# Kernel tuning notes

Measured on AMD Instinct MI355X. Metric: run time of the kernel, lower is better.

The kernel has to match this reference:

```python
import jax, jax.numpy as jnp
import numpy as np
from jax.scipy.special import logsumexp

N_ALPHA = 8192
N_BETA = 8192
N_LAYERS = 16


def setup_inputs() -> dict:
    key = jax.random.key(0)
    k1, k2, k3 = jax.random.split(key, 3)
    alpha = jax.random.uniform(k1, (N_ALPHA,), jnp.float32, 1e-3, 1.0)
    alpha = alpha / alpha.sum()
    beta = jax.random.uniform(k2, (N_BETA,), jnp.float32, 1e-3, 1.0)
    beta = beta / beta.sum()
    C = jax.random.uniform(k3, (N_ALPHA, N_BETA), jnp.float32, 0.0, 1.0)
    eps = jnp.float32(0.1)
    return {"alpha": alpha, "beta": beta, "C": C, "eps": eps}


def reference(alpha, beta, C, eps):
    # Log-domain Sinkhorn iterations (tol=None -> run all n_layers).
    log_alpha = jnp.log(alpha)
    log_beta = jnp.log(beta)

    def step(carry, _):
        _, g = carry
        # log_dot_exp(C, g, eps): logsumexp over n_beta axis of (-C + g[None,:]) / eps
        f = eps * (log_alpha - logsumexp((g[None, :] - C) / eps, axis=-1))
        # log_dot_exp(C.T, f, eps): logsumexp over n_alpha axis of (-C + f[:,None]) / eps
        g_new = eps * (log_beta - logsumexp((f[:, None] - C) / eps, axis=0))
        return (f, g_new), None

    init = (jnp.zeros_like(alpha), jnp.zeros_like(beta))
    (f, g), _ = jax.lax.scan(step, init, None, length=N_LAYERS)
    return f, g
```

## Files before the change

kernel.cpp:

```cpp
#include <hip/hip_runtime.h>

#define NA 8192
#define NB 8192
#define N_LAYERS 16
#define ROWS_PER_VC 64
#define N_VC (NA / ROWS_PER_VC)

typedef _Float16 half_t;
typedef _Float16 half8_t __attribute__((ext_vector_type(8)));
typedef float float4_t __attribute__((ext_vector_type(4)));

template <bool WRITE_E>
__global__ __launch_bounds__(256) void sink_u_first(
    const float* __restrict__ C, const float* __restrict__ alpha,
    const float* __restrict__ d_eps, half_t* __restrict__ E,
    float* __restrict__ u)
{
    const int row = blockIdx.x;
    const int t = threadIdx.x;
    const float inv_eps = 1.0f / d_eps[0];
    const float4_t* Crow = (const float4_t*)(C + (size_t)row * NB);
    half8_t* Erow = (half8_t*)(E + (size_t)row * NB);

    float s = 0.0f;
#pragma unroll
    for (int k = 0; k < 4; ++k) {
        const int g = k * 256 + t;
        float4_t c0 = Crow[2 * g];
        float4_t c1 = Crow[2 * g + 1];
        float e0 = __expf(-c0.x * inv_eps);
        float e1 = __expf(-c0.y * inv_eps);
        float e2 = __expf(-c0.z * inv_eps);
        float e3 = __expf(-c0.w * inv_eps);
        float e4 = __expf(-c1.x * inv_eps);
        float e5 = __expf(-c1.y * inv_eps);
        float e6 = __expf(-c1.z * inv_eps);
        float e7 = __expf(-c1.w * inv_eps);
        if (WRITE_E) {
            half8_t h;
            h[0] = (_Float16)e0; h[1] = (_Float16)e1;
            h[2] = (_Float16)e2; h[3] = (_Float16)e3;
            h[4] = (_Float16)e4; h[5] = (_Float16)e5;
            h[6] = (_Float16)e6; h[7] = (_Float16)e7;
            Erow[g] = h;
        }
        s += ((e0 + e1) + (e2 + e3)) + ((e4 + e5) + (e6 + e7));
    }

    __shared__ float sm[256];
    sm[t] = s;
    __syncthreads();
    for (int off = 128; off > 0; off >>= 1) {
        if (t < off) sm[t] += sm[t + off];
        __syncthreads();
    }
    if (t == 0) u[row] = alpha[row] / sm[0];
}

template <bool USE_E>
__global__ __launch_bounds__(256) void sink_u_step(
    const void* __restrict__ mat, const float* __restrict__ v,
    const float* __restrict__ alpha, const float* __restrict__ d_eps,
    float* __restrict__ u)
{
    const int row = blockIdx.x;
    const int t = threadIdx.x;
    const float4_t* vv = (const float4_t*)v;
    float s = 0.0f;

    if (USE_E) {
        const half8_t* Erow = (const half8_t*)mat + (size_t)row * (NB / 8);
#pragma unroll
        for (int k = 0; k < 4; ++k) {
            const int g = k * 256 + t;
            half8_t e = Erow[g];
            float4_t w0 = vv[2 * g], w1 = vv[2 * g + 1];
            s += (float)e[0] * w0.x + (float)e[1] * w0.y +
                 (float)e[2] * w0.z + (float)e[3] * w0.w;
            s += (float)e[4] * w1.x + (float)e[5] * w1.y +
                 (float)e[6] * w1.z + (float)e[7] * w1.w;
        }
    } else {
        const float inv_eps = 1.0f / d_eps[0];
        const float4_t* Crow = (const float4_t*)mat + (size_t)row * (NB / 4);
#pragma unroll
        for (int k = 0; k < 8; ++k) {
            const int g = k * 256 + t;
            float4_t c = Crow[g];
            float4_t w = vv[g];
            s += __expf(-c.x * inv_eps) * w.x + __expf(-c.y * inv_eps) * w.y +
                 __expf(-c.z * inv_eps) * w.z + __expf(-c.w * inv_eps) * w.w;
        }
    }

    __shared__ float sm[256];
    sm[t] = s;
    __syncthreads();
    for (int off = 128; off > 0; off >>= 1) {
        if (t < off) sm[t] += sm[t + off];
        __syncthreads();
    }
    if (t == 0) u[row] = alpha[row] / sm[0];
}

template <bool USE_E>
__global__ __launch_bounds__(256) void sink_v_partial(
    const void* __restrict__ mat, const float* __restrict__ u,
    const float* __restrict__ d_eps, float* __restrict__ partial)
{
    const int cc = blockIdx.x;
    const int rc = blockIdx.y;
    const int t = threadIdx.x;
    const int row0 = rc * ROWS_PER_VC;

    float acc[8];
#pragma unroll
    for (int k = 0; k < 8; ++k) acc[k] = 0.0f;

    if (USE_E) {
        const half8_t* Eb = (const half8_t*)mat;
        const int g = cc * 256 + t;
#pragma unroll 8
        for (int r = 0; r < ROWS_PER_VC; ++r) {
            const float ur = u[row0 + r];
            half8_t e = Eb[(size_t)(row0 + r) * (NB / 8) + g];
#pragma unroll
            for (int k = 0; k < 8; ++k) acc[k] += ur * (float)e[k];
        }
    } else {
        const float inv_eps = 1.0f / d_eps[0];
        const float4_t* Cb = (const float4_t*)mat;
        const int g = (cc * 256 + t) * 2;
#pragma unroll 4
        for (int r = 0; r < ROWS_PER_VC; ++r) {
            const float ur = u[row0 + r];
            float4_t c0 = Cb[(size_t)(row0 + r) * (NB / 4) + g];
            float4_t c1 = Cb[(size_t)(row0 + r) * (NB / 4) + g + 1];
            acc[0] += ur * __expf(-c0.x * inv_eps);
            acc[1] += ur * __expf(-c0.y * inv_eps);
            acc[2] += ur * __expf(-c0.z * inv_eps);
            acc[3] += ur * __expf(-c0.w * inv_eps);
            acc[4] += ur * __expf(-c1.x * inv_eps);
            acc[5] += ur * __expf(-c1.y * inv_eps);
            acc[6] += ur * __expf(-c1.z * inv_eps);
            acc[7] += ur * __expf(-c1.w * inv_eps);
        }
    }

    float4_t o0 = {acc[0], acc[1], acc[2], acc[3]};
    float4_t o1 = {acc[4], acc[5], acc[6], acc[7]};
    float4_t* p = (float4_t*)(partial + (size_t)rc * NB + (size_t)(cc * 256 + t) * 8);
    p[0] = o0;
    p[1] = o1;
}

__global__ __launch_bounds__(256) void sink_v_combine(
    const float* __restrict__ partial, const float* __restrict__ beta,
    float* __restrict__ v)
{
    const int col = blockIdx.x * 256 + threadIdx.x;
    float s = 0.0f;
#pragma unroll 8
    for (int rc = 0; rc < N_VC; ++rc) s += partial[(size_t)rc * NB + col];
    v[col] = beta[col] / s;
}

__global__ __launch_bounds__(256) void sink_finalize(
    const float* __restrict__ u, const float* __restrict__ v,
    const float* __restrict__ d_eps, float* __restrict__ out)
{
    const int i = blockIdx.x * 256 + threadIdx.x;
    const float eps = d_eps[0];
    if (i < NA) {
        out[i] = eps * logf(u[i]);
    } else if (i < NA + NB) {
        out[i] = eps * logf(v[i - NA]);
    }
}

extern "C" void kernel_launch(void* const* d_in, const int* in_sizes, int n_in,
                              void* d_out, int out_size, void* d_ws, size_t ws_size,
                              hipStream_t stream)
{
    const float* alpha = (const float*)d_in[0];
    const float* beta  = (const float*)d_in[1];
    const float* C     = (const float*)d_in[2];
    const float* d_eps = (const float*)d_in[3];
    float* out = (float*)d_out;

    const size_t eBytes = (size_t)NA * NB * sizeof(half_t);
    const size_t pBytes = (size_t)N_VC * NB * sizeof(float);
    const size_t vecBytes = (size_t)NA * sizeof(float);

    char* ws = (char*)d_ws;
    const bool useE = ws_size >= eBytes + pBytes + 2 * vecBytes;

    size_t off = 0;
    half_t* E = nullptr;
    if (useE) { E = (half_t*)ws; off += eBytes; }
    float* partial = (float*)(ws + off); off += pBytes;
    float* u = (float*)(ws + off); off += vecBytes;
    float* v = (float*)(ws + off); off += vecBytes;

    const dim3 blk(256);
    const dim3 gridRow(NA);
    const dim3 gridVP(NB / 2048, N_VC);
    const dim3 gridVC(NB / 256);

    for (int layer = 0; layer < N_LAYERS; ++layer) {
        if (layer == 0) {
            if (useE)
                sink_u_first<true><<<gridRow, blk, 0, stream>>>(C, alpha, d_eps, E, u);
            else
                sink_u_first<false><<<gridRow, blk, 0, stream>>>(C, alpha, d_eps, nullptr, u);
        } else {
            if (useE)
                sink_u_step<true><<<gridRow, blk, 0, stream>>>(E, v, alpha, d_eps, u);
            else
                sink_u_step<false><<<gridRow, blk, 0, stream>>>(C, v, alpha, d_eps, u);
        }
        if (useE)
            sink_v_partial<true><<<gridVP, blk, 0, stream>>>(E, u, d_eps, partial);
        else
            sink_v_partial<false><<<gridVP, blk, 0, stream>>>(C, u, d_eps, partial);
        sink_v_combine<<<gridVC, blk, 0, stream>>>(partial, beta, v);
    }
    sink_finalize<<<dim3((NA + NB) / 256), blk, 0, stream>>>(u, v, d_eps, out);
}
```

Baseline: 1.166 ms.

## Fuse all Sinkhorn layers into one cooperative persistent kernel with grid syncs

Replaces the roughly 49 separate kernel launches with a single cooperative kernel of 512 blocks that runs every layer and uses grid.sync between phases. It also reworks the row-reduction phase so each wave handles 4 rows with shuffle reductions, which reuses the v loads across rows. The combine stage is parallelised with a shared-memory split. The aim is to remove launch and inter-kernel gaps, at the cost of grid-wide barriers and lower occupancy with only 512 resident blocks.

```diff
diff --git a/kernel.cpp b/kernel.cpp
--- a/kernel.cpp
+++ b/kernel.cpp
@@ -1,8 +1,13 @@
 #include <hip/hip_runtime.h>
+#include <hip/hip_cooperative_groups.h>
+
+namespace cg = cooperative_groups;
 
 #define NA 8192
 #define NB 8192
 #define N_LAYERS 16
+#define NBLK 512
+#define NTHR 256
 #define ROWS_PER_VC 64
 #define N_VC (NA / ROWS_PER_VC)
 
@@ -10,43 +15,222 @@
 typedef _Float16 half8_t __attribute__((ext_vector_type(8)));
 typedef float float4_t __attribute__((ext_vector_type(4)));
 
-template <bool WRITE_E>
-__global__ __launch_bounds__(256) void sink_u_first(
+__device__ __forceinline__ float dot8(half8_t e, float4_t w0, float4_t w1) {
+    return ((float)e[0] * w0.x + (float)e[1] * w0.y) +
+           ((float)e[2] * w0.z + (float)e[3] * w0.w) +
+           ((float)e[4] * w1.x + (float)e[5] * w1.y) +
+           ((float)e[6] * w1.z + (float)e[7] * w1.w);
+}
+
+__device__ __forceinline__ float wave_sum(float a) {
+#pragma unroll
+    for (int off = 32; off > 0; off >>= 1)
+        a += __shfl_down(a, off, 64);
+    return a;
+}
+
+__global__ __launch_bounds__(NTHR, 2) void sink_all(
     const float* __restrict__ C, const float* __restrict__ alpha,
-    const float* __restrict__ d_eps, half_t* __restrict__ E,
-    float* __restrict__ u)
+    const float* __restrict__ beta, const float* __restrict__ d_eps,
+    half_t* __restrict__ E, float* __restrict__ u, float* __restrict__ v,
+    float* __restrict__ partial, float* __restrict__ out)
+{
+    cg::grid_group grid = cg::this_grid();
+    const int b = blockIdx.x;
+    const int t = threadIdx.x;
+    const int wave = t >> 6;
+    const int lane = t & 63;
+    const float eps = d_eps[0];
+    const float inv_eps = 1.0f / eps;
+
+    __shared__ float sm[16][17];
+
+    {
+        const int r0 = b * 16 + wave * 4;
+        const float4_t* C0 = (const float4_t*)(C + (size_t)(r0 + 0) * NB);
+        const float4_t* C1 = (const float4_t*)(C + (size_t)(r0 + 1) * NB);
+        const float4_t* C2 = (const float4_t*)(C + (size_t)(r0 + 2) * NB);
+        const float4_t* C3 = (const float4_t*)(C + (size_t)(r0 + 3) * NB);
+        half8_t* E0 = (half8_t*)(E + (size_t)(r0 + 0) * NB);
+        half8_t* E1 = (half8_t*)(E + (size_t)(r0 + 1) * NB);
+        half8_t* E2 = (half8_t*)(E + (size_t)(r0 + 2) * NB);
+        half8_t* E3 = (half8_t*)(E + (size_t)(r0 + 3) * NB);
+        float a0 = 0.f, a1 = 0.f, a2 = 0.f, a3 = 0.f;
+
+#pragma unroll 2
+        for (int k = 0; k < 16; ++k) {
+            const int g = k * 64 + lane;
+            {
+                float4_t c0 = C0[2 * g], c1 = C0[2 * g + 1];
+                half8_t h;
+                float e0 = __expf(-c0.x * inv_eps), e1 = __expf(-c0.y * inv_eps);
+                float e2 = __expf(-c0.z * inv_eps), e3 = __expf(-c0.w * inv_eps);
+                float e4 = __expf(-c1.x * inv_eps), e5 = __expf(-c1.y * inv_eps);
+                float e6 = __expf(-c1.z * inv_eps), e7 = __expf(-c1.w * inv_eps);
+                h[0] = (_Float16)e0; h[1] = (_Float16)e1; h[2] = (_Float16)e2; h[3] = (_Float16)e3;
+                h[4] = (_Float16)e4; h[5] = (_Float16)e5; h[6] = (_Float16)e6; h[7] = (_Float16)e7;
+                E0[g] = h;
+                a0 += ((e0 + e1) + (e2 + e3)) + ((e4 + e5) + (e6 + e7));
+            }
+            {
+                float4_t c0 = C1[2 * g], c1 = C1[2 * g + 1];
+                half8_t h;
+                float e0 = __expf(-c0.x * inv_eps), e1 = __expf(-c0.y * inv_eps);
+                float e2 = __expf(-c0.z * inv_eps), e3 = __expf(-c0.w * inv_eps);
+                float e4 = __expf(-c1.x * inv_eps), e5 = __expf(-c1.y * inv_eps);
+                float e6 = __expf(-c1.z * inv_eps), e7 = __expf(-c1.w * inv_eps);
+                h[0] = (_Float16)e0; h[1] = (_Float16)e1; h[2] = (_Float16)e2; h[3] = (_Float16)e3;
+                h[4] = (_Float16)e4; h[5] = (_Float16)e5; h[6] = (_Float16)e6; h[7] = (_Float16)e7;
+                E1[g] = h;
+                a1 += ((e0 + e1) + (e2 + e3)) + ((e4 + e5) + (e6 + e7));
+            }
+            {
+                float4_t c0 = C2[2 * g], c1 = C2[2 * g + 1];
+                half8_t h;
+                float e0 = __expf(-c0.x * inv_eps), e1 = __expf(-c0.y * inv_eps);
+                float e2 = __expf(-c0.z * inv_eps), e3 = __expf(-c0.w * inv_eps);
+                float e4 = __expf(-c1.x * inv_eps), e5 = __expf(-c1.y * inv_eps);
+                float e6 = __expf(-c1.z * inv_eps), e7 = __expf(-c1.w * inv_eps);
+                h[0] = (_Float16)e0; h[1] = (_Float16)e1; h[2] = (_Float16)e2; h[3] = (_Float16)e3;
+                h[4] = (_Float16)e4; h[5] = (_Float16)e5; h[6] = (_Float16)e6; h[7] = (_Float16)e7;
+                E2[g] = h;
+                a2 += ((e0 + e1) + (e2 + e3)) + ((e4 + e5) + (e6 + e7));
+            }
+            {
+                float4_t c0 = C3[2 * g], c1 = C3[2 * g + 1];
+                half8_t h;
+                float e0 = __expf(-c0.x * inv_eps), e1 = __expf(-c0.y * inv_eps);
+                float e2 = __expf(-c0.z * inv_eps), e3 = __expf(-c0.w * inv_eps);
+                float e4 = __expf(-c1.x * inv_eps), e5 = __expf(-c1.y * inv_eps);
+                float e6 = __expf(-c1.z * inv_eps), e7 = __expf(-c1.w * inv_eps);
+                h[0] = (_Float16)e0; h[1] = (_Float16)e1; h[2] = (_Float16)e2; h[3] = (_Float16)e3;
+                h[4] = (_Float16)e4; h[5] = (_Float16)e5; h[6] = (_Float16)e6; h[7] = (_Float16)e7;
+                E3[g] = h;
+                a3 += ((e0 + e1) + (e2 + e3)) + ((e4 + e5) + (e6 + e7));
+            }
+        }
+        a0 = wave_sum(a0); a1 = wave_sum(a1); a2 = wave_sum(a2); a3 = wave_sum(a3);
+        if (lane == 0) {
+            u[r0 + 0] = alpha[r0 + 0] / a0;
+            u[r0 + 1] = alpha[r0 + 1] / a1;
+            u[r0 + 2] = alpha[r0 + 2] / a2;
+            u[r0 + 3] = alpha[r0 + 3] / a3;
+        }
+    }
+    grid.sync();
+
+    for (int layer = 0; layer < N_LAYERS; ++layer) {
+        {
+            const int cc = b & 3;
+            const int rc = b >> 2;
+            const int row0 = rc * ROWS_PER_VC;
+            const int g = cc * 256 + t;
+            const half8_t* Eb = (const half8_t*)E;
+
+            float acc[8];
+#pragma unroll
+            for (int k = 0; k < 8; ++k) acc[k] = 0.0f;
+
+#pragma unroll 8
+            for (int r = 0; r < ROWS_PER_VC; ++r) {
+                const float ur = u[row0 + r];
+                half8_t e = Eb[(size_t)(row0 + r) * (NB / 8) + g];
+#pragma unroll
+                for (int k = 0; k < 8; ++k) acc[k] += ur * (float)e[k];
+            }
+            float4_t o0 = {acc[0], acc[1], acc[2], acc[3]};
+            float4_t o1 = {acc[4], acc[5], acc[6], acc[7]};
+            float4_t* p = (float4_t*)(partial + (size_t)rc * NB + (size_t)g * 8);
+            p[0] = o0;
+            p[1] = o1;
+        }
+        grid.sync();
+
+        {
+            const int ci = t & 15;
+            const int grp = t >> 4;
+            const int col = b * 16 + ci;
+            float s = 0.0f;
+#pragma unroll
+            for (int i = 0; i < 8; ++i)
+                s += partial[(size_t)(grp * 8 + i) * NB + col];
+            sm[ci][grp] = s;
+            __syncthreads();
+            if (grp == 0) {
+                float tot = 0.0f;
+#pragma unroll
+                for (int i = 0; i < 16; ++i) tot += sm[ci][i];
+                v[col] = beta[col] / tot;
+            }
+            __syncthreads();
+        }
+        grid.sync();
+
+        if (layer == N_LAYERS - 1) break;
+
+        {
+            const int r0 = b * 16 + wave * 4;
+            const half8_t* E0 = (const half8_t*)(E + (size_t)(r0 + 0) * NB);
+            const half8_t* E1 = (const half8_t*)(E + (size_t)(r0 + 1) * NB);
+            const half8_t* E2 = (const half8_t*)(E + (size_t)(r0 + 2) * NB);
+            const half8_t* E3 = (const half8_t*)(E + (size_t)(r0 + 3) * NB);
+            const float4_t* vv = (const float4_t*)v;
+            float a0 = 0.f, a1 = 0.f, a2 = 0.f, a3 = 0.f;
+
+#pragma unroll 4
+            for (int k = 0; k < 16; ++k) {
+                const int g = k * 64 + lane;
+                float4_t w0 = vv[2 * g];
+                float4_t w1 = vv[2 * g + 1];
+                half8_t e0 = E0[g];
+                half8_t e1 = E1[g];
+                half8_t e2 = E2[g];
+                half8_t e3 = E3[g];
+                a0 += dot8(e0, w0, w1);
+                a1 += dot8(e1, w0, w1);
+                a2 += dot8(e2, w0, w1);
+                a3 += dot8(e3, w0, w1);
+            }
+            a0 = wave_sum(a0); a1 = wave_sum(a1); a2 = wave_sum(a2); a3 = wave_sum(a3);
+            if (lane == 0) {
+                u[r0 + 0] = alpha[r0 + 0] / a0;
+                u[r0 + 1] = alpha[r0 + 1] / a1;
+                u[r0 + 2] = alpha[r0 + 2] / a2;
+                u[r0 + 3] = alpha[r0 + 3] / a3;
+            }
+        }
+        grid.sync();
+    }
+
+    {
+        const int i = b * NTHR + t;
+        if (i < NA) {
+            out[i] = eps * __logf(u[i]);
+        } else if (i < NA + NB) {
+            out[i] = eps * __logf(v[i - NA]);
+        }
+    }
+}
+
+__global__ __launch_bounds__(256) void fb_u_step(
+    const float* __restrict__ C, const float* __restrict__ v,
+    const float* __restrict__ alpha, const float* __restrict__ d_eps,
+    float* __restrict__ u, int first)
 {
     const int row = blockIdx.x;
     const int t = threadIdx.x;
     const float inv_eps = 1.0f / d_eps[0];
     const float4_t* Crow = (const float4_t*)(C + (size_t)row * NB);
-    half8_t* Erow = (half8_t*)(E + (size_t)row * NB);
-
+    const float4_t* vv = (const float4_t*)v;
     float s = 0.0f;
 #pragma unroll
-    for (int k = 0; k < 4; ++k) {
+    for (int k = 0; k < 8; ++k) {
         const int g = k * 256 + t;
-        float4_t c0 = Crow[2 * g];
-        float4_t c1 = Crow[2 * g + 1];
-        float e0 = __expf(-c0.x * inv_eps);
-        float e1 = __expf(-c0.y * inv_eps);
-        float e2 = __expf(-c0.z * inv_eps);
-        float e3 = __expf(-c0.w * inv_eps);
-        float e4 = __expf(-c1.x * inv_eps);
-        float e5 = __expf(-c1.y * inv_eps);
-        float e6 = __expf(-c1.z * inv_eps);
-        float e7 = __expf(-c1.w * inv_eps);
-        if (WRITE_E) {
-            half8_t h;
-            h[0] = (_Float16)e0; h[1] = (_Float16)e1;
-            h[2] = (_Float16)e2; h[3] = (_Float16)e3;
-            h[4] = (_Float16)e4; h[5] = (_Float16)e5;
-            h[6] = (_Float16)e6; h[7] = (_Float16)e7;
-            Erow[g] = h;
-        }
-        s += ((e0 + e1) + (e2 + e3)) + ((e4 + e5) + (e6 + e7));
-    }
-
+        float4_t c = Crow[g];
+        float4_t w = first ? float4_t{1.f, 1.f, 1.f, 1.f} : vv[g];
+        s += __expf(-c.x * inv_eps) * w.x + __expf(-c.y * inv_eps) * w.y +
+             __expf(-c.z * inv_eps) * w.z + __expf(-c.w * inv_eps) * w.w;
+    }
     __shared__ float sm[256];
     sm[t] = s;
     __syncthreads();
@@ -57,96 +241,34 @@
     if (t == 0) u[row] = alpha[row] / sm[0];
 }
 
-template <bool USE_E>
-__global__ __launch_bounds__(256) void sink_u_step(
-    const void* __restrict__ mat, const float* __restrict__ v,
-    const float* __restrict__ alpha, const float* __restrict__ d_eps,
-    float* __restrict__ u)
-{
-    const int row = blockIdx.x;
-    const int t = threadIdx.x;
-    const float4_t* vv = (const float4_t*)v;
-    float s = 0.0f;
-
-    if (USE_E) {
-        const half8_t* Erow = (const half8_t*)mat + (size_t)row * (NB / 8);
-#pragma unroll
-        for (int k = 0; k < 4; ++k) {
-            const int g = k * 256 + t;
-            half8_t e = Erow[g];
-            float4_t w0 = vv[2 * g], w1 = vv[2 * g + 1];
-            s += (float)e[0] * w0.x + (float)e[1] * w0.y +
-                 (float)e[2] * w0.z + (float)e[3] * w0.w;
-            s += (float)e[4] * w1.x + (float)e[5] * w1.y +
-                 (float)e[6] * w1.z + (float)e[7] * w1.w;
-        }
-    } else {
-        const float inv_eps = 1.0f / d_eps[0];
-        const float4_t* Crow = (const float4_t*)mat + (size_t)row * (NB / 4);
-#pragma unroll
-        for (int k = 0; k < 8; ++k) {
-            const int g = k * 256 + t;
-            float4_t c = Crow[g];
-            float4_t w = vv[g];
-            s += __expf(-c.x * inv_eps) * w.x + __expf(-c.y * inv_eps) * w.y +
-                 __expf(-c.z * inv_eps) * w.z + __expf(-c.w * inv_eps) * w.w;
-        }
-    }
-
-    __shared__ float sm[256];
-    sm[t] = s;
-    __syncthreads();
-    for (int off = 128; off > 0; off >>= 1) {
-        if (t < off) sm[t] += sm[t + off];
-        __syncthreads();
-    }
-    if (t == 0) u[row] = alpha[row] / sm[0];
-}
-
-template <bool USE_E>
-__global__ __launch_bounds__(256) void sink_v_partial(
-    const void* __restrict__ mat, const float* __restrict__ u,
+__global__ __launch_bounds__(256) void fb_v_partial(
+    const float* __restrict__ C, const float* __restrict__ u,
     const float* __restrict__ d_eps, float* __restrict__ partial)
 {
     const int cc = blockIdx.x;
     const int rc = blockIdx.y;
     const int t = threadIdx.x;
     const int row0 = rc * ROWS_PER_VC;
-
+    const float inv_eps = 1.0f / d_eps[0];
+    const float4_t* Cb = (const float4_t*)C;
+    const int g = (cc * 256 + t) * 2;
     float acc[8];
 #pragma unroll
     for (int k = 0; k < 8; ++k) acc[k] = 0.0f;
-
-    if (USE_E) {
-        const half8_t* Eb = (const half8_t*)mat;
-        const int g = cc * 256 + t;
-#pragma unroll 8
-        for (int r = 0; r < ROWS_PER_VC; ++r) {
-            const float ur = u[row0 + r];
-            half8_t e = Eb[(size_t)(row0 + r) * (NB / 8) + g];
-#pragma unroll
-            for (int k = 0; k < 8; ++k) acc[k] += ur * (float)e[k];
-        }
-    } else {
-        const float inv_eps = 1.0f / d_eps[0];
-        const float4_t* Cb = (const float4_t*)mat;
-        const int g = (cc * 256 + t) * 2;
 #pragma unroll 4
-        for (int r = 0; r < ROWS_PER_VC; ++r) {
-            const float ur = u[row0 + r];
-            float4_t c0 = Cb[(size_t)(row0 + r) * (NB / 4) + g];
-            float4_t c1 = Cb[(size_t)(row0 + r) * (NB / 4) + g + 1];
-            acc[0] += ur * __expf(-c0.x * inv_eps);
-            acc[1] += ur * __expf(-c0.y * inv_eps);
-            acc[2] += ur * __expf(-c0.z * inv_eps);
-            acc[3] += ur * __expf(-c0.w * inv_eps);
-            acc[4] += ur * __expf(-c1.x * inv_eps);
-            acc[5] += ur * __expf(-c1.y * inv_eps);
-            acc[6] += ur * __expf(-c1.z * inv_eps);
-            acc[7] += ur * __expf(-c1.w * inv_eps);
-        }
-    }
-
+    for (int r = 0; r < ROWS_PER_VC; ++r) {
+        const float ur = u[row0 + r];
+        float4_t c0 = Cb[(size_t)(row0 + r) * (NB / 4) + g];
+        float4_t c1 = Cb[(size_t)(row0 + r) * (NB / 4) + g + 1];
+        acc[0] += ur * __expf(-c0.x * inv_eps);
+        acc[1] += ur * __expf(-c0.y * inv_eps);
+        acc[2] += ur * __expf(-c0.z * inv_eps);
+        acc[3] += ur * __expf(-c0.w * inv_eps);
+        acc[4] += ur * __expf(-c1.x * inv_eps);
+        acc[5] += ur * __expf(-c1.y * inv_eps);
+        acc[6] += ur * __expf(-c1.z * inv_eps);
+        acc[7] += ur * __expf(-c1.w * inv_eps);
+    }
     float4_t o0 = {acc[0], acc[1], acc[2], acc[3]};
     float4_t o1 = {acc[4], acc[5], acc[6], acc[7]};
     float4_t* p = (float4_t*)(partial + (size_t)rc * NB + (size_t)(cc * 256 + t) * 8);
@@ -154,7 +276,7 @@
     p[1] = o1;
 }
 
-__global__ __launch_bounds__(256) void sink_v_combine(
+__global__ __launch_bounds__(256) void fb_v_combine(
     const float* __restrict__ partial, const float* __restrict__ beta,
     float* __restrict__ v)
 {
@@ -165,17 +287,14 @@
     v[col] = beta[col] / s;
 }
 
-__global__ __launch_bounds__(256) void sink_finalize(
+__global__ __launch_bounds__(256) void fb_finalize(
     const float* __restrict__ u, const float* __restrict__ v,
     const float* __restrict__ d_eps, float* __restrict__ out)
 {
     const int i = blockIdx.x * 256 + threadIdx.x;
     const float eps = d_eps[0];
-    if (i < NA) {
-        out[i] = eps * logf(u[i]);
-    } else if (i < NA + NB) {
-        out[i] = eps * logf(v[i - NA]);
-    }
+    if (i < NA) out[i] = eps * logf(u[i]);
+    else if (i < NA + NB) out[i] = eps * logf(v[i - NA]);
 }
 
 extern "C" void kernel_launch(void* const* d_in, const int* in_sizes, int n_in,
@@ -195,35 +314,30 @@
     char* ws = (char*)d_ws;
     const bool useE = ws_size >= eBytes + pBytes + 2 * vecBytes;
 
-    size_t off = 0;
-    half_t* E = nullptr;
-    if (useE) { E = (half_t*)ws; off += eBytes; }
-    float* partial = (float*)(ws + off); off += pBytes;
-    float* u = (float*)(ws + off); off += vecBytes;
-    float* v = (float*)(ws + off); off += vecBytes;
-
-    const dim3 blk(256);
-    const dim3 gridRow(NA);
-    const dim3 gridVP(NB / 2048, N_VC);
-    const dim3 gridVC(NB / 256);
-
-    for (int layer = 0; layer < N_LAYERS; ++layer) {
-        if (layer == 0) {
-            if (useE)
-                sink_u_first<true><<<gridRow, blk, 0, stream>>>(C, alpha, d_eps, E, u);
-            else
-                sink_u_first<false><<<gridRow, blk, 0, stream>>>(C, alpha, d_eps, nullptr, u);
-        } else {
-            if (useE)
-                sink_u_step<true><<<gridRow, blk, 0, stream>>>(E, v, alpha, d_eps, u);
-            else
-                sink_u_step<false><<<gridRow, blk, 0, stream>>>(C, v, alpha, d_eps, u);
-        }
-        if (useE)
-            sink_v_partial<true><<<gridVP, blk, 0, stream>>>(E, u, d_eps, partial);
-        else
-            sink_v_partial<false><<<gridVP, blk, 0, stream>>>(C, u, d_eps, partial);
-        sink_v_combine<<<gridVC, blk, 0, stream>>>(partial, beta, v);
-    }
-    sink_finalize<<<dim3((NA + NB) / 256), blk, 0, stream>>>(u, v, d_eps, out);
-}
+    if (useE) {
+        half_t* E = (half_t*)ws;
+        float* partial = (float*)(ws + eBytes);
+        float* u = (float*)(ws + eBytes + pBytes);
+        float* v = (float*)(ws + eBytes + pBytes + vecBytes);
+
+        void* args[] = {(void*)&C, (void*)&alpha, (void*)&beta, (void*)&d_eps,
+                        (void*)&E, (void*)&u, (void*)&v, (void*)&partial,
+                        (void*)&out};
+        hipLaunchCooperativeKernel((const void*)sink_all, dim3(NBLK), dim3(NTHR),
+                                   args, 0, stream);
+    } else {
+        float* partial = (float*)ws;
+        float* u = (float*)(ws + pBytes);
+        float* v = (float*)(ws + pBytes + vecBytes);
+        const dim3 blk(256);
+        const dim3 gridRow(NA);
+        const dim3 gridVP(NB / 2048, N_VC);
+        for (int layer = 0; layer < N_LAYERS; ++layer) {
+            fb_u_step<<<gridRow, blk, 0, stream>>>(C, v, alpha, d_eps, u,
+                                                   layer == 0 ? 1 : 0);
+            fb_v_partial<<<gridVP, blk, 0, stream>>>(C, u, d_eps, partial);
+            fb_v_combine<<<dim3(NB / 256), blk, 0, stream>>>(partial, beta, v);
+        }
+        fb_finalize<<<dim3((NA + NB) / 256), blk, 0, stream>>>(u, v, d_eps, out);
+    }
+}
```

Result: slower. 3.880 ms (+232.8%).

## Fuse u-step and v-partial into one per-row-chunk kernel reusing E rows

Applied to the files above, without the earlier changes.

Each block now owns 16 rows. It computes u for those rows from the fp16 kernel matrix E, with v staged in LDS, and then immediately computes the column partial sums for the same rows while they are likely still in cache. This aims to avoid a second full read of E from HBM per layer. The finalize step is folded into the last layer's kernels. In exchange the partial buffer grows to 512 chunks, so the combine kernel reads four times more partial data. Each block also uses 32KB of LDS for v, which may limit occupancy.

```diff
diff --git a/kernel.cpp b/kernel.cpp
--- a/kernel.cpp
+++ b/kernel.cpp
@@ -3,50 +3,164 @@
 #define NA 8192
 #define NB 8192
 #define N_LAYERS 16
-#define ROWS_PER_VC 64
-#define N_VC (NA / ROWS_PER_VC)
+#define RPC 16
+#define N_CH (NA / RPC)
+#define FB_RPC 64
+#define FB_NCH (NA / FB_RPC)
 
 typedef _Float16 half_t;
 typedef _Float16 half8_t __attribute__((ext_vector_type(8)));
 typedef float float4_t __attribute__((ext_vector_type(4)));
 
-template <bool WRITE_E>
-__global__ __launch_bounds__(256) void sink_u_first(
-    const float* __restrict__ C, const float* __restrict__ alpha,
-    const float* __restrict__ d_eps, half_t* __restrict__ E,
-    float* __restrict__ u)
+__device__ __forceinline__ float dot8(half8_t e, float4_t w0, float4_t w1) {
+    return (((float)e[0] * w0.x + (float)e[1] * w0.y) +
+            ((float)e[2] * w0.z + (float)e[3] * w0.w)) +
+           (((float)e[4] * w1.x + (float)e[5] * w1.y) +
+            ((float)e[6] * w1.z + (float)e[7] * w1.w));
+}
+
+__device__ __forceinline__ float wave_sum(float a) {
+#pragma unroll
+    for (int off = 32; off > 0; off >>= 1)
+        a += __shfl_down(a, off, 64);
+    return a;
+}
+
+template <bool FIRST, bool LAST>
+__global__ __launch_bounds__(256) void sink_layer(
+    const float* __restrict__ C, half_t* __restrict__ E,
+    const float* __restrict__ v, const float* __restrict__ alpha,
+    const float* __restrict__ d_eps, float* __restrict__ u,
+    float* __restrict__ partial, float* __restrict__ out)
+{
+    const int b = blockIdx.x;
+    const int t = threadIdx.x;
+    const int wave = t >> 6;
+    const int lane = t & 63;
+    const int row0 = b * RPC;
+    const float eps = d_eps[0];
+    const float inv_eps = 1.0f / eps;
+
+    __shared__ float v_s[NB];
+    __shared__ float u_s[RPC];
+
+    if (!FIRST) {
+        const float4_t* vv = (const float4_t*)v;
+        float4_t* vs4 = (float4_t*)v_s;
+#pragma unroll
+        for (int k = 0; k < 8; ++k) vs4[k * 256 + t] = vv[k * 256 + t];
+        __syncthreads();
+    }
+
+#pragma unroll
+    for (int rr = 0; rr < RPC / 4; ++rr) {
+        const int r = row0 + wave * (RPC / 4) + rr;
+        float acc = 0.0f;
+        if (FIRST) {
+            const float4_t* Crow = (const float4_t*)(C + (size_t)r * NB);
+            half8_t* Erow = (half8_t*)(E + (size_t)r * NB);
+#pragma unroll 2
+            for (int k = 0; k < 16; ++k) {
+                const int g = k * 64 + lane;
+                float4_t c0 = Crow[2 * g], c1 = Crow[2 * g + 1];
+                float e0 = __expf(-c0.x * inv_eps), e1 = __expf(-c0.y * inv_eps);
+                float e2 = __expf(-c0.z * inv_eps), e3 = __expf(-c0.w * inv_eps);
+                float e4 = __expf(-c1.x * inv_eps), e5 = __expf(-c1.y * inv_eps);
+                float e6 = __expf(-c1.z * inv_eps), e7 = __expf(-c1.w * inv_eps);
+                half8_t h;
+                h[0] = (_Float16)e0; h[1] = (_Float16)e1;
+                h[2] = (_Float16)e2; h[3] = (_Float16)e3;
+                h[4] = (_Float16)e4; h[5] = (_Float16)e5;
+                h[6] = (_Float16)e6; h[7] = (_Float16)e7;
+                Erow[g] = h;
+                acc += ((e0 + e1) + (e2 + e3)) + ((e4 + e5) + (e6 + e7));
+            }
+        } else {
+            const half8_t* Erow = (const half8_t*)E + (size_t)r * (NB / 8);
+            const float4_t* vs4 = (const float4_t*)v_s;
+#pragma unroll 4
+            for (int k = 0; k < 16; ++k) {
+                const int g = k * 64 + lane;
+                half8_t e = Erow[g];
+                acc += dot8(e, vs4[2 * g], vs4[2 * g + 1]);
+            }
+        }
+        acc = wave_sum(acc);
+        if (lane == 0) {
+            const float uu = alpha[r] / acc;
+            u_s[r - row0] = uu;
+            u[r] = uu;
+            if (LAST) out[r] = eps * __logf(uu);
+        }
+    }
+    __syncthreads();
+
+    const half8_t* Eb = (const half8_t*)E;
+#pragma unroll
+    for (int cc = 0; cc < 4; ++cc) {
+        const int g = cc * 256 + t;
+        float a[8];
+#pragma unroll
+        for (int k = 0; k < 8; ++k) a[k] = 0.0f;
+#pragma unroll
+        for (int r = 0; r < RPC; ++r) {
+            const float ur = u_s[r];
+            half8_t e = Eb[(size_t)(row0 + r) * (NB / 8) + g];
+#pragma unroll
+            for (int k = 0; k < 8; ++k) a[k] += ur * (float)e[k];
+        }
+        float4_t o0 = {a[0], a[1], a[2], a[3]};
+        float4_t o1 = {a[4], a[5], a[6], a[7]};
+        float4_t* p = (float4_t*)(partial + (size_t)b * NB + (size_t)g * 8);
+        p[0] = o0;
+        p[1] = o1;
+    }
+}
+
+template <bool LAST>
+__global__ __launch_bounds__(256) void sink_combine(
+    const float* __restrict__ partial, const float* __restrict__ beta,
+    const float* __restrict__ d_eps, float* __restrict__ v,
+    float* __restrict__ out)
+{
+    const int lane = threadIdx.x & 63;
+    const int w = threadIdx.x >> 6;
+    const int col = blockIdx.x * 64 + lane;
+    float s = 0.0f;
+#pragma unroll 8
+    for (int ch = w * (N_CH / 4); ch < (w + 1) * (N_CH / 4); ++ch)
+        s += partial[(size_t)ch * NB + col];
+    __shared__ float red[4][64];
+    red[w][lane] = s;
+    __syncthreads();
+    if (w == 0) {
+        const float tot = (red[0][lane] + red[1][lane]) +
+                          (red[2][lane] + red[3][lane]);
+        const float vv = beta[col] / tot;
+        v[col] = vv;
+        if (LAST) out[NA + col] = d_eps[0] * __logf(vv);
+    }
+}
+
+__global__ __launch_bounds__(256) void fb_u_step(
+    const float* __restrict__ C, const float* __restrict__ v,
+    const float* __restrict__ alpha, const float* __restrict__ d_eps,
+    float* __restrict__ u, int first)
 {
     const int row = blockIdx.x;
     const int t = threadIdx.x;
     const float inv_eps = 1.0f / d_eps[0];
     const float4_t* Crow = (const float4_t*)(C + (size_t)row * NB);
-    half8_t* Erow = (half8_t*)(E + (size_t)row * NB);
-
+    const float4_t* vv = (const float4_t*)v;
     float s = 0.0f;
 #pragma unroll
-    for (int k = 0; k < 4; ++k) {
+    for (int k = 0; k < 8; ++k) {
         const int g = k * 256 + t;
-        float4_t c0 = Crow[2 * g];
-        float4_t c1 = Crow[2 * g + 1];
-        float e0 = __expf(-c0.x * inv_eps);
-        float e1 = __expf(-c0.y * inv_eps);
-        float e2 = __expf(-c0.z * inv_eps);
-        float e3 = __expf(-c0.w * inv_eps);
-        float e4 = __expf(-c1.x * inv_eps);
-        float e5 = __expf(-c1.y * inv_eps);
-        float e6 = __expf(-c1.z * inv_eps);
-        float e7 = __expf(-c1.w * inv_eps);
-        if (WRITE_E) {
-            half8_t h;
-            h[0] = (_Float16)e0; h[1] = (_Float16)e1;
-            h[2] = (_Float16)e2; h[3] = (_Float16)e3;
-            h[4] = (_Float16)e4; h[5] = (_Float16)e5;
-            h[6] = (_Float16)e6; h[7] = (_Float16)e7;
-            Erow[g] = h;
-        }
-        s += ((e0 + e1) + (e2 + e3)) + ((e4 + e5) + (e6 + e7));
-    }
-
+        float4_t c = Crow[g];
+        float4_t w = first ? float4_t{1.f, 1.f, 1.f, 1.f} : vv[g];
+        s += __expf(-c.x * inv_eps) * w.x + __expf(-c.y * inv_eps) * w.y +
+             __expf(-c.z * inv_eps) * w.z + __expf(-c.w * inv_eps) * w.w;
+    }
     __shared__ float sm[256];
     sm[t] = s;
     __syncthreads();
@@ -57,96 +171,34 @@
     if (t == 0) u[row] = alpha[row] / sm[0];
 }
 
-template <bool USE_E>
-__global__ __launch_bounds__(256) void sink_u_step(
-    const void* __restrict__ mat, const float* __restrict__ v,
-    const float* __restrict__ alpha, const float* __restrict__ d_eps,
-    float* __restrict__ u)
-{
-    const int row = blockIdx.x;
-    const int t = threadIdx.x;
-    const float4_t* vv = (const float4_t*)v;
-    float s = 0.0f;
-
-    if (USE_E) {
-        const half8_t* Erow = (const half8_t*)mat + (size_t)row * (NB / 8);
-#pragma unroll
-        for (int k = 0; k < 4; ++k) {
-            const int g = k * 256 + t;
-            half8_t e = Erow[g];
-            float4_t w0 = vv[2 * g], w1 = vv[2 * g + 1];
-            s += (float)e[0] * w0.x + (float)e[1] * w0.y +
-                 (float)e[2] * w0.z + (float)e[3] * w0.w;
-            s += (float)e[4] * w1.x + (float)e[5] * w1.y +
-                 (float)e[6] * w1.z + (float)e[7] * w1.w;
-        }
-    } else {
-        const float inv_eps = 1.0f / d_eps[0];
-        const float4_t* Crow = (const float4_t*)mat + (size_t)row * (NB / 4);
-#pragma unroll
-        for (int k = 0; k < 8; ++k) {
-            const int g = k * 256 + t;
-            float4_t c = Crow[g];
-            float4_t w = vv[g];
-            s += __expf(-c.x * inv_eps) * w.x + __expf(-c.y * inv_eps) * w.y +
-                 __expf(-c.z * inv_eps) * w.z + __expf(-c.w * inv_eps) * w.w;
-        }
-    }
-
-    __shared__ float sm[256];
-    sm[t] = s;
-    __syncthreads();
-    for (int off = 128; off > 0; off >>= 1) {
-        if (t < off) sm[t] += sm[t + off];
-        __syncthreads();
-    }
-    if (t == 0) u[row] = alpha[row] / sm[0];
-}
-
-template <bool USE_E>
-__global__ __launch_bounds__(256) void sink_v_partial(
-    const void* __restrict__ mat, const float* __restrict__ u,
+__global__ __launch_bounds__(256) void fb_v_partial(
+    const float* __restrict__ C, const float* __restrict__ u,
     const float* __restrict__ d_eps, float* __restrict__ partial)
 {
     const int cc = blockIdx.x;
     const int rc = blockIdx.y;
     const int t = threadIdx.x;
-    const int row0 = rc * ROWS_PER_VC;
-
+    const int row0 = rc * FB_RPC;
+    const float inv_eps = 1.0f / d_eps[0];
+    const float4_t* Cb = (const float4_t*)C;
+    const int g = (cc * 256 + t) * 2;
     float acc[8];
 #pragma unroll
     for (int k = 0; k < 8; ++k) acc[k] = 0.0f;
-
-    if (USE_E) {
-        const half8_t* Eb = (const half8_t*)mat;
-        const int g = cc * 256 + t;
-#pragma unroll 8
-        for (int r = 0; r < ROWS_PER_VC; ++r) {
-            const float ur = u[row0 + r];
-            half8_t e = Eb[(size_t)(row0 + r) * (NB / 8) + g];
-#pragma unroll
-            for (int k = 0; k < 8; ++k) acc[k] += ur * (float)e[k];
-        }
-    } else {
-        const float inv_eps = 1.0f / d_eps[0];
-        const float4_t* Cb = (const float4_t*)mat;
-        const int g = (cc * 256 + t) * 2;
 #pragma unroll 4
-        for (int r = 0; r < ROWS_PER_VC; ++r) {
-            const float ur = u[row0 + r];
-            float4_t c0 = Cb[(size_t)(row0 + r) * (NB / 4) + g];
-            float4_t c1 = Cb[(size_t)(row0 + r) * (NB / 4) + g + 1];
-            acc[0] += ur * __expf(-c0.x * inv_eps);
-            acc[1] += ur * __expf(-c0.y * inv_eps);
-            acc[2] += ur * __expf(-c0.z * inv_eps);
-            acc[3] += ur * __expf(-c0.w * inv_eps);
-            acc[4] += ur * __expf(-c1.x * inv_eps);
-            acc[5] += ur * __expf(-c1.y * inv_eps);
-            acc[6] += ur * __expf(-c1.z * inv_eps);
-            acc[7] += ur * __expf(-c1.w * inv_eps);
-        }
-    }
-
+    for (int r = 0; r < FB_RPC; ++r) {
+        const float ur = u[row0 + r];
+        float4_t c0 = Cb[(size_t)(row0 + r) * (NB / 4) + g];
+        float4_t c1 = Cb[(size_t)(row0 + r) * (NB / 4) + g + 1];
+        acc[0] += ur * __expf(-c0.x * inv_eps);
+        acc[1] += ur * __expf(-c0.y * inv_eps);
+        acc[2] += ur * __expf(-c0.z * inv_eps);
+        acc[3] += ur * __expf(-c0.w * inv_eps);
+        acc[4] += ur * __expf(-c1.x * inv_eps);
+        acc[5] += ur * __expf(-c1.y * inv_eps);
+        acc[6] += ur * __expf(-c1.z * inv_eps);
+        acc[7] += ur * __expf(-c1.w * inv_eps);
+    }
     float4_t o0 = {acc[0], acc[1], acc[2], acc[3]};
     float4_t o1 = {acc[4], acc[5], acc[6], acc[7]};
     float4_t* p = (float4_t*)(partial + (size_t)rc * NB + (size_t)(cc * 256 + t) * 8);
@@ -154,28 +206,25 @@
     p[1] = o1;
 }
 
-__global__ __launch_bounds__(256) void sink_v_combine(
+__global__ __launch_bounds__(256) void fb_v_combine(
     const float* __restrict__ partial, const float* __restrict__ beta,
     float* __restrict__ v)
 {
     const int col = blockIdx.x * 256 + threadIdx.x;
     float s = 0.0f;
 #pragma unroll 8
-    for (int rc = 0; rc < N_VC; ++rc) s += partial[(size_t)rc * NB + col];
+    for (int rc = 0; rc < FB_NCH; ++rc) s += partial[(size_t)rc * NB + col];
     v[col] = beta[col] / s;
 }
 
-__global__ __launch_bounds__(256) void sink_finalize(
+__global__ __launch_bounds__(256) void fb_finalize(
     const float* __restrict__ u, const float* __restrict__ v,
     const float* __restrict__ d_eps, float* __restrict__ out)
 {
     const int i = blockIdx.x * 256 + threadIdx.x;
     const float eps = d_eps[0];
-    if (i < NA) {
-        out[i] = eps * logf(u[i]);
-    } else if (i < NA + NB) {
-        out[i] = eps * logf(v[i - NA]);
-    }
+    if (i < NA) out[i] = eps * logf(u[i]);
+    else if (i < NA + NB) out[i] = eps * logf(v[i - NA]);
 }
 
 extern "C" void kernel_launch(void* const* d_in, const int* in_sizes, int n_in,
@@ -189,41 +238,52 @@
     float* out = (float*)d_out;
 
     const size_t eBytes = (size_t)NA * NB * sizeof(half_t);
-    const size_t pBytes = (size_t)N_VC * NB * sizeof(float);
+    const size_t pBytes = (size_t)N_CH * NB * sizeof(float);
     const size_t vecBytes = (size_t)NA * sizeof(float);
 
     char* ws = (char*)d_ws;
     const bool useE = ws_size >= eBytes + pBytes + 2 * vecBytes;
 
-    size_t off = 0;
-    half_t* E = nullptr;
-    if (useE) { E = (half_t*)ws; off += eBytes; }
-    float* partial = (float*)(ws + off); off += pBytes;
-    float* u = (float*)(ws + off); off += vecBytes;
-    float* v = (float*)(ws + off); off += vecBytes;
-
     const dim3 blk(256);
-    const dim3 gridRow(NA);
-    const dim3 gridVP(NB / 2048, N_VC);
-    const dim3 gridVC(NB / 256);
-
-    for (int layer = 0; layer < N_LAYERS; ++layer) {
-        if (layer == 0) {
-            if (useE)
-                sink_u_first<true><<<gridRow, blk, 0, stream>>>(C, alpha, d_eps, E, u);
+
+    if (useE) {
+        half_t* E = (half_t*)ws;
+        float* partial = (float*)(ws + eBytes);
+        float* u = (float*)(ws + eBytes + pBytes);
+        float* v = (float*)(ws + eBytes + pBytes + vecBytes);
+
+        for (int layer = 0; layer < N_LAYERS; ++layer) {
+            const bool last = (layer == N_LAYERS - 1);
+            if (layer == 0)
+                sink_layer<true, false><<<dim3(N_CH), blk, 0, stream>>>(
+                    C, E, v, alpha, d_eps, u, partial, out);
+            else if (!last)
+                sink_layer<false, false><<<dim3(N_CH), blk, 0, stream>>>(
+                    C, E, v, alpha, d_eps, u, partial, out);
             else
-                sink_u_first<false><<<gridRow, blk, 0, stream>>>(C, alpha, d_eps, nullptr, u);
-        } else {
-            if (useE)
-                sink_u_step<true><<<gridRow, blk, 0, stream>>>(E, v, alpha, d_eps, u);
+                sink_layer<false, true><<<dim3(N_CH), blk, 0, stream>>>(
+                    C, E, v, alpha, d_eps, u, partial, out);
+
+            if (!last)
+                sink_combine<false><<<dim3(NB / 64), blk, 0, stream>>>(
+                    partial, beta, d_eps, v, out);
             else
-                sink_u_step<false><<<gridRow, blk, 0, stream>>>(C, v, alpha, d_eps, u);
-        }
-        if (useE)
-            sink_v_partial<true><<<gridVP, blk, 0, stream>>>(E, u, d_eps, partial);
-        else
-            sink_v_partial<false><<<gridVP, blk, 0, stream>>>(C, u, d_eps, partial);
-        sink_v_combine<<<gridVC, blk, 0, stream>>>(partial, beta, v);
-    }
-    sink_finalize<<<dim3((NA + NB) / 256), blk, 0, stream>>>(u, v, d_eps, out);
-}
+                sink_combine<true><<<dim3(NB / 64), blk, 0, stream>>>(
+                    partial, beta, d_eps, v, out);
+        }
+    } else {
+        const size_t fbPBytes = (size_t)FB_NCH * NB * sizeof(float);
+        float* partial = (float*)ws;
+        float* u = (float*)(ws + fbPBytes);
+        float* v = (float*)(ws + fbPBytes + vecBytes);
+        const dim3 gridRow(NA);
+        const dim3 gridVP(NB / 2048, FB_NCH);
+        for (int layer = 0; layer < N_LAYERS; ++layer) {
+            fb_u_step<<<gridRow, blk, 0, stream>>>(C, v, alpha, d_eps, u,
+                                                   layer == 0 ? 1 : 0);
+            fb_v_partial<<<gridVP, blk, 0, stream>>>(C, u, d_eps, partial);
+            fb_v_combine<<<dim3(NB / 256), blk, 0, stream>>>(partial, beta, v);
+        }
+        fb_finalize<<<dim3((NA + NB) / 256), blk, 0, stream>>>(u, v, d_eps, out);
+    }
+}
```

Result: slower. 1.243 ms (+6.6%).
